# Kernel optimization log

Hardware: AMD Instinct MI355X
Metric: run time of the kernel (lower is better)

## Reference

```python
import jax, jax.numpy as jnp
import numpy as np

N_NODES = 50000
BETA = 0.5
NEG_SLOPE = 0.2


def gat_conv(x, src, dst, W, a_src, a_dst, b):
    """Single-head GAT-style conv: gather, attend, softmax-per-dst, scatter-sum."""
    h = x @ W                                   # [N, F]
    as_ = h @ a_src                             # [N]
    ad_ = h @ a_dst                             # [N]
    e = jax.nn.leaky_relu(as_[src] + ad_[dst], NEG_SLOPE)  # [E]
    # numerically stable softmax over incoming edges of each dst node
    m = jax.ops.segment_max(e, dst, num_segments=N_NODES)  # [N]
    ex = jnp.exp(e - m[dst])                    # [E]
    denom = jax.ops.segment_sum(ex, dst, num_segments=N_NODES)  # [N]
    w = ex / denom[dst]                         # [E]
    out = jax.ops.segment_sum(w[:, None] * h[src], dst, num_segments=N_NODES)
    return out + b


def setup_inputs() -> dict:
    key = jax.random.key(0)
    ks = jax.random.split(key, 8)
    F_in, F_out = 64, 64
    x = jax.random.normal(ks[0], (N_NODES, F_in), dtype=jnp.float32)
    edge_index = jax.random.randint(ks[1], (2, 1600000), 0, N_NODES, dtype=jnp.int64)
    W = jax.random.normal(ks[2], (F_in, F_in), dtype=jnp.float32) * (1.0 / np.sqrt(F_in))
    a_src = jax.random.normal(ks[3], (F_in,), dtype=jnp.float32) * (1.0 / np.sqrt(F_in))
    a_dst = jax.random.normal(ks[4], (F_in,), dtype=jnp.float32) * (1.0 / np.sqrt(F_in))
    b = jnp.zeros((F_in,), dtype=jnp.float32)
    fc_w = jax.random.normal(ks[5], (F_in, F_out), dtype=jnp.float32) * (1.0 / np.sqrt(F_in))
    fc_b = jnp.zeros((F_out,), dtype=jnp.float32)
    return {"x": x, "edge_index": edge_index, "W": W, "a_src": a_src,
            "a_dst": a_dst, "b": b, "fc_w": fc_w, "fc_b": fc_b}


def reference(x, edge_index, W, a_src, a_dst, b, fc_w, fc_b):
    src, dst = edge_index[0], edge_index[1]
    x1 = BETA * gat_conv(x, src, dst, W, a_src, a_dst, b) + (1.0 - BETA) * x
    x2 = BETA * gat_conv(x1, src, dst, W, a_src, a_dst, b) + (1.0 - BETA) * x
    x3 = BETA * gat_conv(x2, src, dst, W, a_src, a_dst, b) + (1.0 - BETA) * x
    h = x3
    out = x3 @ fc_w + fc_b
    return (out, h)
```

## Files before the change

### kernel.cpp

```cpp
#include <hip/hip_runtime.h>
#include <hip/hip_bf16.h>
#include <math.h>

#define N_NODES 50000
#define FDIM 64
#define BETA 0.5f
#define NEG_SLOPE 0.2f

typedef __attribute__((ext_vector_type(8))) short bf16x8;
typedef __attribute__((ext_vector_type(4))) float f32x4;

__device__ __forceinline__ unsigned short f2bf(float f) {
    unsigned u = __float_as_uint(f);
    unsigned r = (u + 0x7FFFu + ((u >> 16) & 1u)) >> 16;
    return (unsigned short)r;
}
__device__ __forceinline__ float bf2f(unsigned short s) {
    return __uint_as_float((unsigned)s << 16);
}

#define CHUNK 4096
__global__ __launch_bounds__(256) void scatter_pairs(
    const unsigned int* __restrict__ eiu, int* __restrict__ gCursor,
    unsigned int* __restrict__ pairs, int E, int CAP) {
    __shared__ int det;
    __shared__ unsigned int staged[CHUNK];
    __shared__ unsigned short tmpd[CHUNK];
    __shared__ int hist[256], sc[256], lbase[256], gbase[256], lcur[256];
    int t = threadIdx.x;
    if (t == 0) det = 0;
    hist[t] = 0;
    __syncthreads();
    int beg = blockIdx.x * CHUNK;
    int end = min(E, beg + CHUNK);
    int n = end - beg;
    {
        int idx = beg + t;
        if (idx < E && eiu[2 * idx + 1] != 0u) atomicOr(&det, 1);
    }
    __syncthreads();
    bool is32 = det != 0;
    for (int i = beg + t; i < end; i += 256) {
        int d = is32 ? (int)eiu[E + i] : (int)eiu[2 * (size_t)(E + i)];
        tmpd[i - beg] = (unsigned short)d;
        atomicAdd(&hist[d >> 8], 1);
    }
    __syncthreads();
    sc[t] = hist[t];
    __syncthreads();
    for (int off = 1; off < 256; off <<= 1) {
        int v = (t >= off) ? sc[t - off] : 0;
        __syncthreads();
        sc[t] += v;
        __syncthreads();
    }
    int excl = sc[t] - hist[t];
    lbase[t] = excl;
    lcur[t] = excl;
    if (hist[t] > 0) gbase[t] = t * CAP + atomicAdd(&gCursor[t], hist[t]);
    __syncthreads();
    for (int i = beg + t; i < end; i += 256) {
        unsigned s = is32 ? eiu[i] : eiu[2 * (size_t)i];
        unsigned td = tmpd[i - beg];
        int b = (int)(td >> 8);
        int lp = atomicAdd(&lcur[b], 1);
        staged[lp] = s | (td << 16);
    }
    __syncthreads();
    for (int j = t; j < n; j += 256) {
        unsigned w = staged[j];
        int b = (int)(w >> 24);
        pairs[gbase[b] + (j - lbase[b])] = w;
    }
}

__global__ __launch_bounds__(1024) void bucket_sort(
    const unsigned int* __restrict__ pairs, const int* __restrict__ gCursor,
    int* __restrict__ offsets, int* __restrict__ srcs, int N, int E, int CAP) {
    __shared__ int scb[256], cnt[256], sc[256], lcur[256];
    __shared__ unsigned short sorted16[16384];
    int b = blockIdx.x, t = threadIdx.x;
    if (t < 256) scb[t] = gCursor[t];
    __syncthreads();
    for (int off = 1; off < 256; off <<= 1) {
        int v = (t < 256 && t >= off) ? scb[t - off] : 0;
        __syncthreads();
        if (t < 256) scb[t] += v;
        __syncthreads();
    }
    int cntb = gCursor[b];
    int beg = scb[b] - cntb;
    int pbase = b * CAP;
    bool useLds = cntb <= 16384;
    if (b == 0 && t == 0) offsets[N] = E;
    if (t < 256) cnt[t] = 0;
    __syncthreads();
    for (int i = t; i < cntb; i += 1024) atomicAdd(&cnt[(pairs[pbase + i] >> 16) & 255u], 1);
    __syncthreads();
    if (t < 256) sc[t] = cnt[t];
    __syncthreads();
    for (int off = 1; off < 256; off <<= 1) {
        int v = (t < 256 && t >= off) ? sc[t - off] : 0;
        __syncthreads();
        if (t < 256) sc[t] += v;
        __syncthreads();
    }
    if (t < 256) {
        int excl = sc[t] - cnt[t];
        int node = (b << 8) + t;
        if (node < N) offsets[node] = beg + excl;
        lcur[t] = excl;
    }
    __syncthreads();
    if (useLds) {
        for (int i = t; i < cntb; i += 1024) {
            unsigned p = pairs[pbase + i];
            int lp = atomicAdd(&lcur[(p >> 16) & 255u], 1);
            sorted16[lp] = (unsigned short)(p & 0xFFFFu);
        }
        __syncthreads();
        for (int j = t; j < cntb; j += 1024) srcs[beg + j] = (int)sorted16[j];
    } else {
        for (int i = t; i < cntb; i += 1024) {
            unsigned p = pairs[pbase + i];
            int lp = atomicAdd(&lcur[(p >> 16) & 255u], 1);
            srcs[beg + lp] = (int)(p & 0xFFFFu);
        }
    }
}

__global__ __launch_bounds__(256) void deg_hist(
    const int* __restrict__ offsets, int* __restrict__ degCnt, int N) {
    __shared__ int h[256];
    h[threadIdx.x] = 0;
    __syncthreads();
    for (int i = blockIdx.x * blockDim.x + threadIdx.x; i < N; i += gridDim.x * blockDim.x) {
        int d = offsets[i + 1] - offsets[i];
        atomicAdd(&h[min(d, 255)], 1);
    }
    __syncthreads();
    if (h[threadIdx.x]) atomicAdd(&degCnt[threadIdx.x], h[threadIdx.x]);
}

__global__ __launch_bounds__(256) void deg_scan(int* degCnt) {
    __shared__ int sc[256];
    int t = threadIdx.x;
    int c = degCnt[t];
    sc[t] = c;
    __syncthreads();
    for (int off = 1; off < 256; off <<= 1) {
        int v = (t >= off) ? sc[t - off] : 0;
        __syncthreads();
        sc[t] += v;
        __syncthreads();
    }
    degCnt[t] = sc[t] - c;
}

#define DCHUNK 2048
__global__ __launch_bounds__(256) void deg_scatter(
    const int* __restrict__ offsets, int* __restrict__ degCnt,
    int* __restrict__ perm, int N) {
    __shared__ int lh[256], lbase[256], lcur[256];
    int t = threadIdx.x;
    int beg = blockIdx.x * DCHUNK;
    int end = min(N, beg + DCHUNK);
    lh[t] = 0;
    lcur[t] = 0;
    __syncthreads();
    for (int i = beg + t; i < end; i += 256) {
        int d = min(offsets[i + 1] - offsets[i], 255);
        atomicAdd(&lh[d], 1);
    }
    __syncthreads();
    if (lh[t] > 0) lbase[t] = atomicAdd(&degCnt[t], lh[t]);
    __syncthreads();
    for (int i = beg + t; i < end; i += 256) {
        int d = min(offsets[i + 1] - offsets[i], 255);
        int r = atomicAdd(&lcur[d], 1);
        perm[lbase[d] + r] = i;
    }
}

__global__ __launch_bounds__(256) void prep_weights(
    const float* __restrict__ W, const float* __restrict__ fcw,
    unsigned short* __restrict__ WTh, unsigned short* __restrict__ WTl,
    unsigned short* __restrict__ FTh, unsigned short* __restrict__ FTl) {
    for (int idx = blockIdx.x * 256 + threadIdx.x; idx < 4096; idx += gridDim.x * 256) {
        int k = idx >> 6, f = idx & 63;
        float w = W[idx];
        unsigned short hi = f2bf(w);
        WTh[f * 64 + k] = hi;
        WTl[f * 64 + k] = f2bf(w - bf2f(hi));
        float w2 = fcw[idx];
        unsigned short hi2 = f2bf(w2);
        FTh[f * 64 + k] = hi2;
        FTl[f * 64 + k] = f2bf(w2 - bf2f(hi2));
    }
}

__global__ __launch_bounds__(256, 4) void transform_mfma(
    const float* __restrict__ x,
    const unsigned short* __restrict__ WTh, const unsigned short* __restrict__ WTl,
    const float* __restrict__ a_src, const float* __restrict__ a_dst,
    const float* __restrict__ bias,
    unsigned short* __restrict__ hb,
    float* __restrict__ fout,
    float* __restrict__ as_, float* __restrict__ ad_, int N) {
    __shared__ __align__(16) unsigned short WThs[64 * 72];
    __shared__ __align__(16) unsigned short WTls[64 * 72];
    int tid = threadIdx.x;
    {
        int row = tid >> 2;
        int ch = (tid & 3) * 16;
        uint4 h0 = ((const uint4*)(WTh + row * 64 + ch))[0];
        uint4 h1 = ((const uint4*)(WTh + row * 64 + ch))[1];
        uint4 l0 = ((const uint4*)(WTl + row * 64 + ch))[0];
        uint4 l1 = ((const uint4*)(WTl + row * 64 + ch))[1];
        *((uint4*)(WThs + row * 72 + ch)) = h0;
        *((uint4*)(WThs + row * 72 + ch + 8)) = h1;
        *((uint4*)(WTls + row * 72 + ch)) = l0;
        *((uint4*)(WTls + row * 72 + ch + 8)) = l1;
    }

    int wid = tid >> 6;
    int lane = tid & 63;
    int col = lane & 15;
    int quad = lane >> 4;
    int mbase = blockIdx.x * 64 + wid * 16;

    bf16x8 Ah[2], Al[2];
    int arow = mbase + col;
    const float* xr = x + (size_t)(arow < N ? arow : 0) * FDIM + quad * 8;
#pragma unroll
    for (int ks = 0; ks < 2; ks++) {
        float4 xa = *(const float4*)(xr + ks * 32);
        float4 xb = *(const float4*)(xr + ks * 32 + 4);
        float xv[8] = {xa.x, xa.y, xa.z, xa.w, xb.x, xb.y, xb.z, xb.w};
#pragma unroll
        for (int e = 0; e < 8; e++) {
            unsigned short hi = f2bf(xv[e]);
            Ah[ks][e] = (short)hi;
            Al[ks][e] = (short)f2bf(xv[e] - bf2f(hi));
        }
    }
    __syncthreads();

    f32x4 acc[4];
#pragma unroll
    for (int ft = 0; ft < 4; ft++) acc[ft] = (f32x4){0.f, 0.f, 0.f, 0.f};

#pragma unroll
    for (int ft = 0; ft < 4; ft++) {
        int f = ft * 16 + col;
#pragma unroll
        for (int ks = 0; ks < 2; ks++) {
            int off = f * 72 + ks * 32 + quad * 8;
            bf16x8 Bh = *(const bf16x8*)(WThs + off);
            bf16x8 Bl = *(const bf16x8*)(WTls + off);
            acc[ft] = __builtin_amdgcn_mfma_f32_16x16x32_bf16(Ah[ks], Bh, acc[ft], 0, 0, 0);
            acc[ft] = __builtin_amdgcn_mfma_f32_16x16x32_bf16(Ah[ks], Bl, acc[ft], 0, 0, 0);
            acc[ft] = __builtin_amdgcn_mfma_f32_16x16x32_bf16(Al[ks], Bh, acc[ft], 0, 0, 0);
        }
    }

    if (fout) {
#pragma unroll
        for (int ft = 0; ft < 4; ft++) {
            int f = ft * 16 + col;
            float bv = bias ? bias[f] : 0.f;
#pragma unroll
            for (int r = 0; r < 4; r++) {
                int node = mbase + quad * 4 + r;
                if (node < N) fout[(size_t)node * FDIM + f] = acc[ft][r] + bv;
            }
        }
    }
    if (hb) {
#pragma unroll
        for (int ft = 0; ft < 4; ft++) {
            int f = ft * 16 + col;
#pragma unroll
            for (int r = 0; r < 4; r++) {
                int node = mbase + quad * 4 + r;
                if (node < N) hb[(size_t)node * FDIM + f] = f2bf(acc[ft][r]);
            }
        }
    }
    if (as_) {
        float asv[4], adv[4];
#pragma unroll
        for (int ft = 0; ft < 4; ft++) {
            asv[ft] = a_src[ft * 16 + col];
            adv[ft] = a_dst[ft * 16 + col];
        }
#pragma unroll
        for (int r = 0; r < 4; r++) {
            float pa = 0.f, pd = 0.f;
#pragma unroll
            for (int ft = 0; ft < 4; ft++) {
                pa = fmaf(acc[ft][r], asv[ft], pa);
                pd = fmaf(acc[ft][r], adv[ft], pd);
            }
#pragma unroll
            for (int off = 1; off <= 8; off <<= 1) {
                pa += __shfl_xor(pa, off, 64);
                pd += __shfl_xor(pd, off, 64);
            }
            int node = mbase + quad * 4 + r;
            if (col == 0 && node < N) { as_[node] = pa; ad_[node] = pd; }
        }
    }
}

__device__ __forceinline__ void fma8(float* acc, float ex, const uint4& hv) {
    acc[0] = fmaf(ex, __uint_as_float(hv.x << 16), acc[0]);
    acc[1] = fmaf(ex, __uint_as_float(hv.x & 0xFFFF0000u), acc[1]);
    acc[2] = fmaf(ex, __uint_as_float(hv.y << 16), acc[2]);
    acc[3] = fmaf(ex, __uint_as_float(hv.y & 0xFFFF0000u), acc[3]);
    acc[4] = fmaf(ex, __uint_as_float(hv.z << 16), acc[4]);
    acc[5] = fmaf(ex, __uint_as_float(hv.z & 0xFFFF0000u), acc[5]);
    acc[6] = fmaf(ex, __uint_as_float(hv.w << 16), acc[6]);
    acc[7] = fmaf(ex, __uint_as_float(hv.w & 0xFFFF0000u), acc[7]);
}

__global__ __launch_bounds__(256) void gat_gather(
    const unsigned short* __restrict__ hb,
    const float* __restrict__ as_, const float* __restrict__ ad_,
    const int* __restrict__ offsets, const int* __restrict__ srcs,
    const int* __restrict__ perm,
    const float* __restrict__ bvec, const float* __restrict__ x0,
    float* __restrict__ xout, int N) {
    int wid = (blockIdx.x * blockDim.x + threadIdx.x) >> 6;
    int lane = threadIdx.x & 63;
    int g = lane >> 3;
    int q = lane & 7;
    int ni = wid * 8 + g;
    bool active = ni < N;
    int node = active ? perm[ni] : 0;
    int beg = active ? offsets[node] : 0;
    int end = active ? offsets[node + 1] : 0;
    float adv = active ? ad_[node] : 0.f;
    int mx = end - beg;
    mx = max(mx, __shfl_xor(mx, 8, 64));
    mx = max(mx, __shfl_xor(mx, 16, 64));
    mx = max(mx, __shfl_xor(mx, 32, 64));

    float acc[8];
#pragma unroll
    for (int k = 0; k < 8; k++) acc[k] = 0.f;
    float denom = 0.f;
    const unsigned short* hq = hb + (q << 3);

#define LRELU_EXP(E_) __expf((E_) > 0.f ? (E_) : NEG_SLOPE * (E_))

    for (int st = 0; st < mx; st += 4) {
        int i0 = beg + st;
        bool v0 = i0 < end, v1 = i0 + 1 < end, v2 = i0 + 2 < end, v3 = i0 + 3 < end;
        int a0 = v0 ? i0 : 0;
        int a1 = v1 ? i0 + 1 : 0;
        int a2 = v2 ? i0 + 2 : 0;
        int a3 = v3 ? i0 + 3 : 0;
        int s0 = srcs[a0];
        int s1 = srcs[a1];
        int s2 = srcs[a2];
        int s3 = srcs[a3];
        uint4 hv0 = *(const uint4*)(hq + ((size_t)s0 << 6));
        uint4 hv1 = *(const uint4*)(hq + ((size_t)s1 << 6));
        uint4 hv2 = *(const uint4*)(hq + ((size_t)s2 << 6));
        uint4 hv3 = *(const uint4*)(hq + ((size_t)s3 << 6));
        float e0 = as_[s0] + adv;
        float e1 = as_[s1] + adv;
        float e2 = as_[s2] + adv;
        float e3 = as_[s3] + adv;
        float ex0 = v0 ? LRELU_EXP(e0) : 0.f;
        float ex1 = v1 ? LRELU_EXP(e1) : 0.f;
        float ex2 = v2 ? LRELU_EXP(e2) : 0.f;
        float ex3 = v3 ? LRELU_EXP(e3) : 0.f;
        denom += (ex0 + ex1) + (ex2 + ex3);
        fma8(acc, ex0, hv0);
        fma8(acc, ex1, hv1);
        fma8(acc, ex2, hv2);
        fma8(acc, ex3, hv3);
    }
#undef LRELU_EXP

    if (active) {
        float inv = denom > 0.f ? 1.f / denom : 0.f;
        int fb = q * 8;
        f32x4 b0 = *(const f32x4*)(bvec + fb);
        f32x4 b1 = *(const f32x4*)(bvec + fb + 4);
        const float* x0r = x0 + (size_t)node * FDIM + fb;
        f32x4 x0a = *(const f32x4*)(x0r);
        f32x4 x0b = *(const f32x4*)(x0r + 4);
        f32x4 o0, o1;
        o0.x = BETA * (acc[0] * inv + b0.x) + (1.f - BETA) * x0a.x;
        o0.y = BETA * (acc[1] * inv + b0.y) + (1.f - BETA) * x0a.y;
        o0.z = BETA * (acc[2] * inv + b0.z) + (1.f - BETA) * x0a.z;
        o0.w = BETA * (acc[3] * inv + b0.w) + (1.f - BETA) * x0a.w;
        o1.x = BETA * (acc[4] * inv + b1.x) + (1.f - BETA) * x0b.x;
        o1.y = BETA * (acc[5] * inv + b1.y) + (1.f - BETA) * x0b.y;
        o1.z = BETA * (acc[6] * inv + b1.z) + (1.f - BETA) * x0b.z;
        o1.w = BETA * (acc[7] * inv + b1.w) + (1.f - BETA) * x0b.w;
        float* xr = xout + (size_t)node * FDIM + fb;
        *(f32x4*)(xr) = o0;
        *(f32x4*)(xr + 4) = o1;
    }
}

extern "C" void kernel_launch(void* const* d_in, const int* in_sizes, int n_in,
                              void* d_out, int out_size, void* d_ws, size_t ws_size,
                              hipStream_t stream) {
    const int N = N_NODES;
    const int E = in_sizes[1] / 2;
    const int NB = (N + 255) >> 8;
    const int CAP = (((E / N) * 256) * 2 + 1023) & ~1023;

    const float* x     = (const float*)d_in[0];
    const void*  ei    = d_in[1];
    const float* W     = (const float*)d_in[2];
    const float* a_src = (const float*)d_in[3];
    const float* a_dst = (const float*)d_in[4];
    const float* bvec  = (const float*)d_in[5];
    const float* fc_w  = (const float*)d_in[6];
    const float* fc_b  = (const float*)d_in[7];

    float* out = (float*)d_out;
    float* x3  = out + (size_t)N * FDIM;

    char* p = (char*)d_ws;
    auto alloc = [&](size_t bytes) -> void* {
        void* r = (void*)p;
        p += (bytes + 255) & ~(size_t)255;
        return r;
    };
    int*            gCursor  = (int*)alloc(512 * 4);
    unsigned int*   pairs    = (unsigned int*)alloc((size_t)256 * CAP * 4);
    int*            srcs     = (int*)alloc((size_t)E * 4);
    int*            offsets  = (int*)alloc((size_t)(N + 1) * 4);
    int*            perm     = (int*)alloc((size_t)N * 4);
    float*          as_      = (float*)alloc((size_t)N * 4);
    float*          ad_      = (float*)alloc((size_t)N * 4);
    unsigned short* hbuf     = (unsigned short*)alloc((size_t)N * FDIM * 2);
    float*          xbuf     = (float*)alloc((size_t)N * FDIM * 4);
    unsigned short* WTh      = (unsigned short*)alloc(4096 * 2);
    unsigned short* WTl      = (unsigned short*)alloc(4096 * 2);
    unsigned short* FTh      = (unsigned short*)alloc(4096 * 2);
    unsigned short* FTl      = (unsigned short*)alloc(4096 * 2);
    int* degCnt = gCursor + 256;

    hipMemsetAsync(gCursor, 0, 512 * 4, stream);

    prep_weights<<<16, 256, 0, stream>>>(W, fc_w, WTh, WTl, FTh, FTl);

    scatter_pairs<<<(E + CHUNK - 1) / CHUNK, 256, 0, stream>>>(
        (const unsigned int*)ei, gCursor, pairs, E, CAP);
    bucket_sort<<<NB, 1024, 0, stream>>>(pairs, gCursor, offsets, srcs, N, E, CAP);

    deg_hist<<<64, 256, 0, stream>>>(offsets, degCnt, N);
    deg_scan<<<1, 256, 0, stream>>>(degCnt);
    deg_scatter<<<(N + DCHUNK - 1) / DCHUNK, 256, 0, stream>>>(offsets, degCnt, perm, N);

    int tgrid = (N + 63) / 64;
    int gwaves = (N + 7) / 8;
    int ggrid = (gwaves + 3) / 4;

    transform_mfma<<<tgrid, 256, 0, stream>>>(x, WTh, WTl, a_src, a_dst, nullptr,
                                              hbuf, nullptr, as_, ad_, N);
    gat_gather<<<ggrid, 256, 0, stream>>>(hbuf, as_, ad_, offsets, srcs, perm,
                                          bvec, x, xbuf, N);
    transform_mfma<<<tgrid, 256, 0, stream>>>(xbuf, WTh, WTl, a_src, a_dst, nullptr,
                                              hbuf, nullptr, as_, ad_, N);
    gat_gather<<<ggrid, 256, 0, stream>>>(hbuf, as_, ad_, offsets, srcs, perm,
                                          bvec, x, xbuf, N);
    transform_mfma<<<tgrid, 256, 0, stream>>>(xbuf, WTh, WTl, a_src, a_dst, nullptr,
                                              hbuf, nullptr, as_, ad_, N);
    gat_gather<<<ggrid, 256, 0, stream>>>(hbuf, as_, ad_, offsets, srcs, perm,
                                          bvec, x, x3, N);
    transform_mfma<<<tgrid, 256, 0, stream>>>(x3, FTh, FTl, nullptr, nullptr, fc_b,
                                              nullptr, out, nullptr, nullptr, N);
}
```

Before: 262.6 us.

## Store CSR sources as u16, fuse degree histogram into bucket sort, unroll gather by 8

Source indices in the CSR array are now stored as 16-bit values, which halves the index traffic in the bucket sort writes and in the three gather passes. The degree histogram is computed inside bucket_sort from the per-node counts already held in shared memory, so the separate deg_hist launch is removed. The gather loop now handles 8 edges per step instead of 4, putting more loads in flight at the cost of extra registers and more wasted lanes on low-degree nodes. The 16-bit index depends on node ids staying below 65536, which holds for N=50000 and was already assumed by the packing in scatter_pairs.

```diff
diff --git a/kernel.cpp b/kernel.cpp
--- a/kernel.cpp
+++ b/kernel.cpp
@@ -76,11 +76,12 @@
 
 __global__ __launch_bounds__(1024) void bucket_sort(
     const unsigned int* __restrict__ pairs, const int* __restrict__ gCursor,
-    int* __restrict__ offsets, int* __restrict__ srcs, int N, int E, int CAP) {
-    __shared__ int scb[256], cnt[256], sc[256], lcur[256];
+    int* __restrict__ offsets, unsigned short* __restrict__ srcs,
+    int* __restrict__ degCnt, int N, int E, int CAP) {
+    __shared__ int scb[256], cnt[256], sc[256], lcur[256], dh[256];
     __shared__ unsigned short sorted16[16384];
     int b = blockIdx.x, t = threadIdx.x;
-    if (t < 256) scb[t] = gCursor[t];
+    if (t < 256) { scb[t] = gCursor[t]; dh[t] = 0; }
     __syncthreads();
     for (int off = 1; off < 256; off <<= 1) {
         int v = (t < 256 && t >= off) ? scb[t - off] : 0;
@@ -97,8 +98,13 @@
     __syncthreads();
     for (int i = t; i < cntb; i += 1024) atomicAdd(&cnt[(pairs[pbase + i] >> 16) & 255u], 1);
     __syncthreads();
-    if (t < 256) sc[t] = cnt[t];
-    __syncthreads();
+    if (t < 256) {
+        sc[t] = cnt[t];
+        int node = (b << 8) + t;
+        if (node < N) atomicAdd(&dh[min(cnt[t], 255)], 1);
+    }
+    __syncthreads();
+    if (t < 256 && dh[t]) atomicAdd(&degCnt[t], dh[t]);
     for (int off = 1; off < 256; off <<= 1) {
         int v = (t < 256 && t >= off) ? sc[t - off] : 0;
         __syncthreads();
@@ -119,27 +125,14 @@
             sorted16[lp] = (unsigned short)(p & 0xFFFFu);
         }
         __syncthreads();
-        for (int j = t; j < cntb; j += 1024) srcs[beg + j] = (int)sorted16[j];
+        for (int j = t; j < cntb; j += 1024) srcs[beg + j] = sorted16[j];
     } else {
         for (int i = t; i < cntb; i += 1024) {
             unsigned p = pairs[pbase + i];
             int lp = atomicAdd(&lcur[(p >> 16) & 255u], 1);
-            srcs[beg + lp] = (int)(p & 0xFFFFu);
-        }
-    }
-}
-
-__global__ __launch_bounds__(256) void deg_hist(
-    const int* __restrict__ offsets, int* __restrict__ degCnt, int N) {
-    __shared__ int h[256];
-    h[threadIdx.x] = 0;
-    __syncthreads();
-    for (int i = blockIdx.x * blockDim.x + threadIdx.x; i < N; i += gridDim.x * blockDim.x) {
-        int d = offsets[i + 1] - offsets[i];
-        atomicAdd(&h[min(d, 255)], 1);
-    }
-    __syncthreads();
-    if (h[threadIdx.x]) atomicAdd(&degCnt[threadIdx.x], h[threadIdx.x]);
+            srcs[beg + lp] = (unsigned short)(p & 0xFFFFu);
+        }
+    }
 }
 
 __global__ __launch_bounds__(256) void deg_scan(int* degCnt) {
@@ -327,7 +320,7 @@
 __global__ __launch_bounds__(256) void gat_gather(
     const unsigned short* __restrict__ hb,
     const float* __restrict__ as_, const float* __restrict__ ad_,
-    const int* __restrict__ offsets, const int* __restrict__ srcs,
+    const int* __restrict__ offsets, const unsigned short* __restrict__ srcs,
     const int* __restrict__ perm,
     const float* __restrict__ bvec, const float* __restrict__ x0,
     float* __restrict__ xout, int N) {
@@ -354,34 +347,27 @@
 
 #define LRELU_EXP(E_) __expf((E_) > 0.f ? (E_) : NEG_SLOPE * (E_))
 
-    for (int st = 0; st < mx; st += 4) {
+    for (int st = 0; st < mx; st += 8) {
         int i0 = beg + st;
-        bool v0 = i0 < end, v1 = i0 + 1 < end, v2 = i0 + 2 < end, v3 = i0 + 3 < end;
-        int a0 = v0 ? i0 : 0;
-        int a1 = v1 ? i0 + 1 : 0;
-        int a2 = v2 ? i0 + 2 : 0;
-        int a3 = v3 ? i0 + 3 : 0;
-        int s0 = srcs[a0];
-        int s1 = srcs[a1];
-        int s2 = srcs[a2];
-        int s3 = srcs[a3];
-        uint4 hv0 = *(const uint4*)(hq + ((size_t)s0 << 6));
-        uint4 hv1 = *(const uint4*)(hq + ((size_t)s1 << 6));
-        uint4 hv2 = *(const uint4*)(hq + ((size_t)s2 << 6));
-        uint4 hv3 = *(const uint4*)(hq + ((size_t)s3 << 6));
-        float e0 = as_[s0] + adv;
-        float e1 = as_[s1] + adv;
-        float e2 = as_[s2] + adv;
-        float e3 = as_[s3] + adv;
-        float ex0 = v0 ? LRELU_EXP(e0) : 0.f;
-        float ex1 = v1 ? LRELU_EXP(e1) : 0.f;
-        float ex2 = v2 ? LRELU_EXP(e2) : 0.f;
-        float ex3 = v3 ? LRELU_EXP(e3) : 0.f;
-        denom += (ex0 + ex1) + (ex2 + ex3);
-        fma8(acc, ex0, hv0);
-        fma8(acc, ex1, hv1);
-        fma8(acc, ex2, hv2);
-        fma8(acc, ex3, hv3);
+        bool v[8];
+        int s[8];
+        uint4 hv[8];
+        float ex[8];
+#pragma unroll
+        for (int k = 0; k < 8; k++) {
+            v[k] = (i0 + k) < end;
+            s[k] = (int)srcs[v[k] ? i0 + k : 0];
+        }
+#pragma unroll
+        for (int k = 0; k < 8; k++) hv[k] = *(const uint4*)(hq + ((size_t)s[k] << 6));
+#pragma unroll
+        for (int k = 0; k < 8; k++) {
+            float e = as_[s[k]] + adv;
+            ex[k] = v[k] ? LRELU_EXP(e) : 0.f;
+            denom += ex[k];
+        }
+#pragma unroll
+        for (int k = 0; k < 8; k++) fma8(acc, ex[k], hv[k]);
     }
 #undef LRELU_EXP
 
@@ -436,7 +422,7 @@
     };
     int*            gCursor  = (int*)alloc(512 * 4);
     unsigned int*   pairs    = (unsigned int*)alloc((size_t)256 * CAP * 4);
-    int*            srcs     = (int*)alloc((size_t)E * 4);
+    unsigned short* srcs     = (unsigned short*)alloc((size_t)E * 2);
     int*            offsets  = (int*)alloc((size_t)(N + 1) * 4);
     int*            perm     = (int*)alloc((size_t)N * 4);
     float*          as_      = (float*)alloc((size_t)N * 4);
@@ -455,9 +441,8 @@
 
     scatter_pairs<<<(E + CHUNK - 1) / CHUNK, 256, 0, stream>>>(
         (const unsigned int*)ei, gCursor, pairs, E, CAP);
-    bucket_sort<<<NB, 1024, 0, stream>>>(pairs, gCursor, offsets, srcs, N, E, CAP);
-
-    deg_hist<<<64, 256, 0, stream>>>(offsets, degCnt, N);
+    bucket_sort<<<NB, 1024, 0, stream>>>(pairs, gCursor, offsets, srcs, degCnt, N, E, CAP);
+
     deg_scan<<<1, 256, 0, stream>>>(degCnt);
     deg_scatter<<<(N + DCHUNK - 1) / DCHUNK, 256, 0, stream>>>(offsets, degCnt, perm, N);
 
```

Result: slower. 280.4 us (+6.8%).
